# Performance work log

Hardware: AMD Instinct MI355X
Metric: run time of the kernel (lower is better)

## Reference

```python
import jax, jax.numpy as jnp
import numpy as np

H = 768          # MODEL_SIZE
N = 16           # SSM state modes (complex, conj-symmetric half)
NUM_LAYERS = 6
NUM_OUTS = 38


def setup_inputs() -> dict:
    key = jax.random.key(0)
    ks = jax.random.split(key, 24)
    B, L = 8, 2048
    scale = 0.02
    x_feat = jax.random.normal(ks[0], (B, L, 8), jnp.float32)
    x_raw = jax.random.normal(ks[1], (B, L, 8), jnp.float32)
    session_ids = jax.random.randint(ks[2], (B,), 0, 32)
    # encoder: Linear(8,H) -> Softsign -> Linear(H,H)
    enc_w1 = jax.random.normal(ks[3], (8, H), jnp.float32) * scale
    enc_b1 = jnp.zeros((H,), jnp.float32)
    enc_w2 = jax.random.normal(ks[4], (H, H), jnp.float32) * scale
    enc_b2 = jnp.zeros((H,), jnp.float32)
    # per-layer S4 params, stacked over NUM_LAYERS
    lo, hi = np.log(1e-3), np.log(1e-1)
    log_dt = lo + (hi - lo) * jax.random.uniform(ks[5], (NUM_LAYERS, H), jnp.float32)
    log_A_real = jnp.log(0.5 * jnp.ones((NUM_LAYERS, H, N), jnp.float32))
    A_imag = jnp.broadcast_to(np.pi * jnp.arange(N, dtype=jnp.float32), (NUM_LAYERS, H, N)) + 0.0
    C_ri = jax.random.normal(ks[6], (NUM_LAYERS, 2, H, N, 2), jnp.float32) * (0.5 ** 0.5)  # bidirectional C (re/im)
    D = jax.random.normal(ks[7], (NUM_LAYERS, H), jnp.float32)
    out_w = jax.random.normal(ks[8], (NUM_LAYERS, 2 * H, H), jnp.float32) * scale  # GLU output linear
    out_b = jnp.zeros((NUM_LAYERS, 2 * H), jnp.float32)
    norm_w = jnp.ones((NUM_LAYERS, H), jnp.float32)
    norm_b = jnp.zeros((NUM_LAYERS, H), jnp.float32)
    wout_w = jax.random.normal(ks[9], (H, NUM_OUTS), jnp.float32) * scale
    wout_b = jnp.zeros((NUM_OUTS,), jnp.float32)
    return dict(x_feat=x_feat, x_raw=x_raw, session_ids=session_ids,
                enc_w1=enc_w1, enc_b1=enc_b1, enc_w2=enc_w2, enc_b2=enc_b2,
                log_dt=log_dt, log_A_real=log_A_real, A_imag=A_imag, C_ri=C_ri,
                D=D, out_w=out_w, out_b=out_b, norm_w=norm_w, norm_b=norm_b,
                wout_w=wout_w, wout_b=wout_b)


def _s4_kernel(log_dt, log_A_real, A_imag, C_ri, L):
    """Bidirectional diagonal SSM conv kernel via ZOH discretization. Returns (2, H, L)."""
    dt = jnp.exp(log_dt)                              # (H,)
    A = (-jnp.exp(log_A_real) + 1j * A_imag).astype(jnp.complex64)   # (H, N)
    dtA = (dt[:, None] * A).astype(jnp.complex64)     # (H, N)
    dB = (jnp.exp(dtA) - 1.0) / A                     # ZOH input discretization (B=1)
    C = (C_ri[..., 0] + 1j * C_ri[..., 1]).astype(jnp.complex64)     # (2, H, N)
    vand = jnp.exp(dtA[:, :, None] * jnp.arange(L, dtype=jnp.float32))  # (H, N, L)
    K = 2.0 * jnp.einsum('chn,hnl->chl', C * dB, vand).real           # conj-symmetry factor
    return K.astype(jnp.float32)


def _s4_layer(x, log_dt, log_A_real, A_imag, C_ri, D, out_w, out_b, norm_w, norm_b):
    """x: (B, L, H) -> (B, L, H). Post-norm S4 block (eval mode, dropout=identity)."""
    B, L, _ = x.shape
    u = x.transpose(0, 2, 1)                          # (B, H, L)
    K = _s4_kernel(log_dt, log_A_real, A_imag, C_ri, L)  # (2, H, L)
    zpad = jnp.zeros((H, L), K.dtype)
    k = (jnp.concatenate([K[0], zpad], -1)
         + jnp.concatenate([zpad, jnp.flip(K[1], -1)], -1))            # (H, 2L) bidirectional kernel
    yf = jnp.fft.irfft(jnp.fft.rfft(u, n=2 * L) * jnp.fft.rfft(k, n=2 * L), n=2 * L)[..., :L]
    y = yf + D[:, None] * u                           # skip connection
    y = jax.nn.gelu(y, approximate=False)
    v = jnp.einsum('dh,bhl->bdl', out_w, y) + out_b[None, :, None]     # (B, 2H, L)
    a, g = jnp.split(v, 2, axis=1)
    z = a * jax.nn.sigmoid(g)                         # GLU
    xr = (z + u).transpose(0, 2, 1)                   # residual, back to (B, L, H)
    mu = xr.mean(-1, keepdims=True)
    var = ((xr - mu) ** 2).mean(-1, keepdims=True)
    return (xr - mu) / jnp.sqrt(var + 1e-5) * norm_w + norm_b          # post-LayerNorm


def reference(x_feat, x_raw, session_ids, enc_w1, enc_b1, enc_w2, enc_b2,
              log_dt, log_A_real, A_imag, C_ri, D, out_w, out_b,
              norm_w, norm_b, wout_w, wout_b):
    x = jax.nn.soft_sign(x_raw @ enc_w1 + enc_b1) @ enc_w2 + enc_b2    # encoder
    for i in range(NUM_LAYERS):
        x = _s4_layer(x, log_dt[i], log_A_real[i], A_imag[i], C_ri[i],
                      D[i], out_w[i], out_b[i], norm_w[i], norm_b[i])
        if i <= 2:
            x = x[:, ::2, :]                          # stride-2 downsample
    return x @ wout_w + wout_b                        # (B, L/8, num_outs)
```

## Files before the change

kernel.cpp:

```cpp
#include <hip/hip_runtime.h>
#include <hip/hip_bf16.h>
#include <math.h>

#define HDIM 768
#define NSTATE 16

typedef __attribute__((ext_vector_type(8))) short bf16x8;
typedef __attribute__((ext_vector_type(4))) float f32x4;
typedef __attribute__((ext_vector_type(4))) unsigned int u32x4;

__device__ __forceinline__ unsigned short f2bf(float f) {
    union { float f; unsigned int u; } v; v.f = f;
    unsigned int r = v.u + 0x7fff + ((v.u >> 16) & 1);
    return (unsigned short)(r >> 16);
}

__global__ void __launch_bounds__(256) wconv_kernel(
    const float* __restrict__ src, unsigned short* __restrict__ dst, int n8)
{
    int t = blockIdx.x * 256 + threadIdx.x;
    if (t >= n8) return;
    const float* s = src + (size_t)t * 8;
    float4 a = *(const float4*)s, b = *(const float4*)(s + 4);
    union { unsigned short us[8]; u32x4 v; } o;
    o.us[0] = f2bf(a.x); o.us[1] = f2bf(a.y); o.us[2] = f2bf(a.z); o.us[3] = f2bf(a.w);
    o.us[4] = f2bf(b.x); o.us[5] = f2bf(b.y); o.us[6] = f2bf(b.z); o.us[7] = f2bf(b.w);
    *(u32x4*)(dst + (size_t)t * 8) = o.v;
}

__global__ void __launch_bounds__(256) w2t_kernel(
    const float* __restrict__ w2, unsigned short* __restrict__ w2t)
{
    int T = blockIdx.x * 256 + threadIdx.x;
    int j = T / 96, kc = T - j * 96;
    union { unsigned short us[8]; u32x4 v; } o;
#pragma unroll
    for (int i = 0; i < 8; ++i)
        o.us[i] = f2bf(w2[(size_t)(kc * 8 + i) * HDIM + j]);
    *(u32x4*)(w2t + (size_t)j * HDIM + kc * 8) = o.v;
}

__global__ void __launch_bounds__(256) hprep_kernel(
    const float* __restrict__ xraw, const float* __restrict__ w1,
    const float* __restrict__ b1, unsigned short* __restrict__ hbf)
{
    __shared__ float w1s[8 * HDIM];
    __shared__ float b1s[HDIM];
    int tid = threadIdx.x;
    for (int p = tid; p < 8 * HDIM; p += 256) w1s[p] = w1[p];
    for (int p = tid; p < HDIM; p += 256) b1s[p] = b1[p];
    __syncthreads();
    int T = blockIdx.x * 256 + tid;
    int r = T / 96, kc = T - r * 96;
    float4 xa = *(const float4*)(xraw + (size_t)r * 8);
    float4 xb = *(const float4*)(xraw + (size_t)r * 8 + 4);
    float xq[8] = {xa.x, xa.y, xa.z, xa.w, xb.x, xb.y, xb.z, xb.w};
    float acc[8];
#pragma unroll
    for (int i = 0; i < 8; ++i) acc[i] = b1s[kc * 8 + i];
#pragma unroll
    for (int q = 0; q < 8; ++q)
#pragma unroll
        for (int i = 0; i < 8; ++i)
            acc[i] = fmaf(xq[q], w1s[q * HDIM + kc * 8 + i], acc[i]);
    union { unsigned short us[8]; u32x4 v; } o;
#pragma unroll
    for (int i = 0; i < 8; ++i) {
        float h = acc[i] / (1.0f + fabsf(acc[i]));
        o.us[i] = f2bf(h);
    }
    *(u32x4*)(hbf + (size_t)r * HDIM + kc * 8) = o.v;
}

__global__ void __launch_bounds__(256) enc_mfma_kernel(
    const unsigned short* __restrict__ w2t,
    const unsigned short* __restrict__ hbf,
    const float* __restrict__ b2,
    float* __restrict__ u0)
{
    __shared__ unsigned short lds[2][192 * 64];
    int tid = threadIdx.x;
    int j0 = blockIdx.x * 64;
    int r0 = blockIdx.y * 128;
    int w = tid >> 6, lane = tid & 63;
    int wj = w >> 1, wl = w & 1;
    f32x4 acc[2][4];
    f32x4 zf = {0.f, 0.f, 0.f, 0.f};
#pragma unroll
    for (int dg = 0; dg < 2; ++dg)
#pragma unroll
        for (int cg = 0; cg < 4; ++cg) acc[dg][cg] = zf;

    u32x4 stg[6];
#define ENC_LOAD(kt) do { int k0_ = (kt) * 64; \
    _Pragma("unroll") for (int s = 0; s < 6; ++s) { \
        int c = s * 256 + tid; int row = c >> 3, m = c & 7; \
        const unsigned short* g = (row < 64) \
            ? (w2t + (size_t)(j0 + row) * HDIM + k0_ + m * 8) \
            : (hbf + (size_t)(r0 + row - 64) * HDIM + k0_ + m * 8); \
        stg[s] = *(const u32x4*)g; } } while (0)
#define ENC_WRITE(bi) do { \
    _Pragma("unroll") for (int s = 0; s < 6; ++s) { \
        int c = s * 256 + tid; int row = c >> 3, m = c & 7; \
        *(u32x4*)&lds[bi][row * 64 + 8 * (m ^ (row & 7))] = stg[s]; } } while (0)

    ENC_LOAD(0); ENC_WRITE(0);
    int cur = 0;
    for (int t = 0; t < 12; ++t) {
        __syncthreads();
        if (t < 11) ENC_LOAD(t + 1);
#pragma unroll
        for (int kh = 0; kh < 2; ++kh) {
            int kg = kh * 4 + (lane >> 4);
            bf16x8 af[2], bfr[4];
#pragma unroll
            for (int dg = 0; dg < 2; ++dg) {
                int rA = wj * 32 + dg * 16 + (lane & 15);
                af[dg] = *(bf16x8*)&lds[cur][rA * 64 + 8 * (kg ^ (rA & 7))];
            }
#pragma unroll
            for (int cg = 0; cg < 4; ++cg) {
                int rB = 64 + wl * 64 + cg * 16 + (lane & 15);
                bfr[cg] = *(bf16x8*)&lds[cur][rB * 64 + 8 * (kg ^ (rB & 7))];
            }
#pragma unroll
            for (int dg = 0; dg < 2; ++dg)
#pragma unroll
                for (int cg = 0; cg < 4; ++cg)
                    acc[dg][cg] = __builtin_amdgcn_mfma_f32_16x16x32_bf16(
                        af[dg], bfr[cg], acc[dg][cg], 0, 0, 0);
        }
        if (t < 11) ENC_WRITE(cur ^ 1);
        cur ^= 1;
    }
    int b = r0 >> 11;
    int l0 = r0 & 2047;
#pragma unroll
    for (int dg = 0; dg < 2; ++dg) {
        int j = j0 + wj * 32 + dg * 16 + ((lane >> 4) << 2);
#pragma unroll
        for (int cg = 0; cg < 4; ++cg) {
            int l = l0 + wl * 64 + cg * 16 + (lane & 15);
#pragma unroll
            for (int i = 0; i < 4; ++i)
                u0[((size_t)(b * HDIM + j + i)) * 2048 + l] = acc[dg][cg][i] + b2[j + i];
        }
    }
#undef ENC_LOAD
#undef ENC_WRITE
}

__global__ void __launch_bounds__(256) glu_mfma_kernel(
    const unsigned short* __restrict__ wbf,
    const unsigned short* __restrict__ yt,
    const float* __restrict__ u,
    const float* __restrict__ ob,
    float* __restrict__ xr,
    int Lk, int ds)
{
    __shared__ unsigned short lds[2][256 * 64];
    int tid = threadIdx.x;
    int d0 = blockIdx.x * 64;
    int l0 = blockIdx.y * 128;
    int b  = blockIdx.z;
    int w = tid >> 6, lane = tid & 63;
    int wd = w >> 1, wl = w & 1;
    f32x4 accA[2][4], accG[2][4];
    f32x4 zf = {0.f, 0.f, 0.f, 0.f};
#pragma unroll
    for (int dg = 0; dg < 2; ++dg)
#pragma unroll
        for (int cg = 0; cg < 4; ++cg) { accA[dg][cg] = zf; accG[dg][cg] = zf; }

    u32x4 stg[8];
#define GLU_LOAD(kt) do { int k0_ = (kt) * 64; \
    _Pragma("unroll") for (int s = 0; s < 8; ++s) { \
        int c = s * 256 + tid; int row = c >> 3, m = c & 7; \
        const unsigned short* g; \
        if (row < 64)       g = wbf + (size_t)(d0 + row) * HDIM + k0_ + m * 8; \
        else if (row < 128) g = wbf + (size_t)(768 + d0 + row - 64) * HDIM + k0_ + m * 8; \
        else g = yt + ((size_t)b * Lk + l0 + row - 128) * HDIM + k0_ + m * 8; \
        stg[s] = *(const u32x4*)g; } } while (0)
#define GLU_WRITE(bi) do { \
    _Pragma("unroll") for (int s = 0; s < 8; ++s) { \
        int c = s * 256 + tid; int row = c >> 3, m = c & 7; \
        *(u32x4*)&lds[bi][row * 64 + 8 * (m ^ (row & 7))] = stg[s]; } } while (0)

    GLU_LOAD(0); GLU_WRITE(0);
    int cur = 0;
    for (int t = 0; t < 12; ++t) {
        __syncthreads();
        if (t < 11) GLU_LOAD(t + 1);
#pragma unroll
        for (int kh = 0; kh < 2; ++kh) {
            int kg = kh * 4 + (lane >> 4);
            bf16x8 aa[2], ag[2], bfr[4];
#pragma unroll
            for (int dg = 0; dg < 2; ++dg) {
                int rA = wd * 32 + dg * 16 + (lane & 15);
                aa[dg] = *(bf16x8*)&lds[cur][rA * 64 + 8 * (kg ^ (rA & 7))];
                int rG = 64 + rA;
                ag[dg] = *(bf16x8*)&lds[cur][rG * 64 + 8 * (kg ^ (rG & 7))];
            }
#pragma unroll
            for (int cg = 0; cg < 4; ++cg) {
                int rB = 128 + wl * 64 + cg * 16 + (lane & 15);
                bfr[cg] = *(bf16x8*)&lds[cur][rB * 64 + 8 * (kg ^ (rB & 7))];
            }
#pragma unroll
            for (int dg = 0; dg < 2; ++dg)
#pragma unroll
                for (int cg = 0; cg < 4; ++cg) {
                    accA[dg][cg] = __builtin_amdgcn_mfma_f32_16x16x32_bf16(
                        aa[dg], bfr[cg], accA[dg][cg], 0, 0, 0);
                    accG[dg][cg] = __builtin_amdgcn_mfma_f32_16x16x32_bf16(
                        ag[dg], bfr[cg], accG[dg][cg], 0, 0, 0);
                }
        }
        if (t < 11) GLU_WRITE(cur ^ 1);
        cur ^= 1;
    }
    size_t L = (size_t)Lk * ds;
#pragma unroll
    for (int dg = 0; dg < 2; ++dg) {
        int d = d0 + wd * 32 + dg * 16 + ((lane >> 4) << 2);
#pragma unroll
        for (int cg = 0; cg < 4; ++cg) {
            int l = l0 + wl * 64 + cg * 16 + (lane & 15);
#pragma unroll
            for (int i = 0; i < 4; ++i) {
                float a = accA[dg][cg][i] + ob[d + i];
                float g = accG[dg][cg][i] + ob[d + i + 768];
                float sg = 1.0f / (1.0f + expf(-g));
                float res = u[((size_t)b * HDIM + d + i) * L + (size_t)l * ds];
                xr[((size_t)b * HDIM + d + i) * Lk + l] = fmaf(a, sg, res);
            }
        }
    }
#undef GLU_LOAD
#undef GLU_WRITE
}

template<int DS>
__global__ void __launch_bounds__(256) ssm_split_kernel(
    const float* __restrict__ u,
    float* __restrict__ yout,
    const float* __restrict__ log_dt,
    const float* __restrict__ log_A_real,
    const float* __restrict__ A_imag,
    const float* __restrict__ C_ri,
    const float* __restrict__ Dp,
    int L, int lognch)
{
    __shared__ float4 tlsv[1024];
    const int KEPT = 32 / DS;
    int tid = threadIdx.x;
    int nch = 1 << lognch;
    int sh  = tid & 1;
    int j   = (tid >> 1) & (nch - 1);
    int rpb = 128 >> lognch;
    int lr  = tid >> (1 + lognch);
    int row = blockIdx.x * rpb + lr;
    int b   = row / HDIM;
    int h   = row - b * HDIM;
    int c0  = j * 32;
    const float* ur = u + (size_t)row * L;
    int Lk = L / DS;

    float zr[8], zi[8], zCr[8], zCi[8], w0r[8], w0i[8], w1r[8], w1i[8];
    float dt = expf(log_dt[h]);
#pragma unroll
    for (int k = 0; k < 8; ++k) {
        int n = sh * 8 + k;
        float Ar = -expf(log_A_real[h * NSTATE + n]);
        float Ai = A_imag[h * NSTATE + n];
        float er = expf(dt * Ar);
        float th = dt * Ai;
        zr[k] = er * cosf(th); zi[k] = er * sinf(th);
        float pr = zr[k], pi = zi[k];
#pragma unroll
        for (int s = 0; s < 5; ++s) {
            float t2 = pr * pr - pi * pi;
            pi = 2.f * pr * pi; pr = t2;
        }
        zCr[k] = pr; zCi[k] = pi;
        float den = Ar * Ar + Ai * Ai;
        float t0 = zr[k] - 1.0f;
        float dBr = (t0 * Ar + zi[k] * Ai) / den;
        float dBi = (zi[k] * Ar - t0 * Ai) / den;
        float C0r = C_ri[((0 * HDIM + h) * NSTATE + n) * 2 + 0];
        float C0i = C_ri[((0 * HDIM + h) * NSTATE + n) * 2 + 1];
        float C1r = C_ri[((1 * HDIM + h) * NSTATE + n) * 2 + 0];
        float C1i = C_ri[((1 * HDIM + h) * NSTATE + n) * 2 + 1];
        w0r[k] = 2.0f * (C0r * dBr - C0i * dBi);
        w0i[k] = 2.0f * (C0r * dBi + C0i * dBr);
        w1r[k] = 2.0f * (C1r * dBr - C1i * dBi);
        w1i[k] = 2.0f * (C1r * dBi + C1i * dBr);
    }
    int myslot = (j * rpb + lr) * 2 + sh;

    {
        float sr_[8] = {}, si_[8] = {};
#pragma unroll 8
        for (int i = 0; i < 32; ++i) {
            float uf = ur[c0 + i];
#pragma unroll
            for (int k = 0; k < 8; ++k) {
                float nr = fmaf(zr[k], sr_[k], fmaf(-zi[k], si_[k], uf));
                si_[k] = fmaf(zr[k], si_[k], zi[k] * sr_[k]);
                sr_[k] = nr;
            }
        }
#pragma unroll
        for (int q = 0; q < 4; ++q)
            tlsv[myslot * 4 + (q ^ (myslot & 3))] =
                make_float4(sr_[2 * q], si_[2 * q], sr_[2 * q + 1], si_[2 * q + 1]);
    }
    __syncthreads();

    float Sr[8] = {}, Si[8] = {};
    for (int i = 0; i < j; ++i) {
        int sl = (i * rpb + lr) * 2 + sh;
        float4 t0v = tlsv[sl * 4 + (0 ^ (sl & 3))];
        float4 t1v = tlsv[sl * 4 + (1 ^ (sl & 3))];
        float4 t2v = tlsv[sl * 4 + (2 ^ (sl & 3))];
        float4 t3v = tlsv[sl * 4 + (3 ^ (sl & 3))];
        float tr[8] = {t0v.x, t0v.z, t1v.x, t1v.z, t2v.x, t2v.z, t3v.x, t3v.z};
        float ti[8] = {t0v.y, t0v.w, t1v.y, t1v.w, t2v.y, t2v.w, t3v.y, t3v.w};
#pragma unroll
        for (int k = 0; k < 8; ++k) {
            float nr = fmaf(zCr[k], Sr[k], fmaf(-zCi[k], Si[k], tr[k]));
            Si[k] = fmaf(zCr[k], Si[k], fmaf(zCi[k], Sr[k], ti[k]));
            Sr[k] = nr;
        }
    }

    float Dh_eff = (sh == 0) ? Dp[h] : 0.0f;
    float cf[KEPT];
#pragma unroll
    for (int i = 0; i < 32; ++i) {
        float uf = ur[c0 + i];
        float ca = 0.f, cb = 0.f;
#pragma unroll
        for (int k = 0; k < 8; ++k) {
            float nr = fmaf(zr[k], Sr[k], fmaf(-zi[k], Si[k], uf));
            Si[k] = fmaf(zr[k], Si[k], zi[k] * Sr[k]);
            Sr[k] = nr;
            float c = fmaf(w0r[k], Sr[k], -w0i[k] * Si[k]);
            if (k & 1) cb += c; else ca += c;
        }
        if ((i & (DS - 1)) == 0)
            cf[i / DS] = fmaf(Dh_eff, uf, ca + cb);
    }
    __syncthreads();

    {
        float sr_[8] = {}, si_[8] = {};
#pragma unroll 8
        for (int m = 0; m < 32; ++m) {
            int idx = c0 + 32 - m;
            float ub = (idx < L) ? ur[idx] : 0.f;
#pragma unroll
            for (int k = 0; k < 8; ++k) {
                float nr = fmaf(zr[k], sr_[k], fmaf(-zi[k], si_[k], ub));
                si_[k] = fmaf(zr[k], si_[k], zi[k] * sr_[k]);
                sr_[k] = nr;
            }
        }
#pragma unroll
        for (int q = 0; q < 4; ++q)
            tlsv[myslot * 4 + (q ^ (myslot & 3))] =
                make_float4(sr_[2 * q], si_[2 * q], sr_[2 * q + 1], si_[2 * q + 1]);
    }
    __syncthreads();

    float Er[8] = {}, Ei[8] = {};
    for (int i = nch - 1; i > j; --i) {
        int sl = (i * rpb + lr) * 2 + sh;
        float4 t0v = tlsv[sl * 4 + (0 ^ (sl & 3))];
        float4 t1v = tlsv[sl * 4 + (1 ^ (sl & 3))];
        float4 t2v = tlsv[sl * 4 + (2 ^ (sl & 3))];
        float4 t3v = tlsv[sl * 4 + (3 ^ (sl & 3))];
        float tr[8] = {t0v.x, t0v.z, t1v.x, t1v.z, t2v.x, t2v.z, t3v.x, t3v.z};
        float ti[8] = {t0v.y, t0v.w, t1v.y, t1v.w, t2v.y, t2v.w, t3v.y, t3v.w};
#pragma unroll
        for (int k = 0; k < 8; ++k) {
            float nr = fmaf(zCr[k], Er[k], fmaf(-zCi[k], Ei[k], tr[k]));
            Ei[k] = fmaf(zCr[k], Ei[k], fmaf(zCi[k], Er[k], ti[k]));
            Er[k] = nr;
        }
    }

    float* yr = yout + (size_t)row * Lk + (c0 / DS);
#pragma unroll
    for (int m = 0; m < 32; ++m) {
        int idx = c0 + 32 - m;
        float ub = (idx < L) ? ur[idx] : 0.f;
#pragma unroll
        for (int k = 0; k < 8; ++k) {
            float nr = fmaf(zr[k], Er[k], fmaf(-zi[k], Ei[k], ub));
            Ei[k] = fmaf(zr[k], Ei[k], zi[k] * Er[k]);
            Er[k] = nr;
        }
        if (((31 - m) & (DS - 1)) == 0) {
            float ca = 0.f, cb = 0.f;
#pragma unroll
            for (int k = 0; k < 8; ++k) {
                float c = fmaf(w1r[k], Er[k], -w1i[k] * Ei[k]);
                if (k & 1) cb += c; else ca += c;
            }
            int k2 = (31 - m) / DS;
            float v = cf[k2] + ca + cb;
            v += __shfl_xor(v, 1, 64);
            if (sh == 0) {
                float g = 0.5f * v * (1.0f + erff(v * 0.70710678118f));
                yr[k2] = g;
            }
        }
    }
}

__global__ void __launch_bounds__(256) ytr_kernel(
    const float* __restrict__ yf, unsigned short* __restrict__ yt, int Lk)
{
    __shared__ float tile[64][65];
    int tid = threadIdx.x;
    int p0 = blockIdx.x * 64;
    int r0 = blockIdx.y * 64;
    int tp = tid & 63, th = tid >> 6;
#pragma unroll
    for (int s = 0; s < 16; ++s) {
        int hh = th * 16 + s;
        tile[hh][tp] = yf[(size_t)(r0 + hh) * Lk + p0 + tp];
    }
    __syncthreads();
    int b = r0 / HDIM, h0 = r0 - b * HDIM;
#pragma unroll
    for (int s = 0; s < 16; ++s) {
        int pp = th * 16 + s;
        yt[((size_t)b * Lk + p0 + pp) * HDIM + h0 + tp] = f2bf(tile[tp][pp]);
    }
}

__global__ void __launch_bounds__(256) ln_kernel(
    const float* __restrict__ x, float* __restrict__ dst,
    const float* __restrict__ nw, const float* __restrict__ nb, int Lk)
{
    __shared__ float ss[16][17], qq[16][17], mus[16], rss[16];
    int tid = threadIdx.x;
    int lo = tid & 15, hg = tid >> 4;
    int b = blockIdx.y;
    int l = blockIdx.x * 16 + lo;
    const float* base = x + (size_t)b * HDIM * Lk + l;
    float s = 0.f, q = 0.f;
    for (int hh = hg; hh < HDIM; hh += 16) {
        float v = base[(size_t)hh * Lk];
        s += v; q = fmaf(v, v, q);
    }
    ss[hg][lo] = s; qq[hg][lo] = q;
    __syncthreads();
    if (hg == 0) {
        float S = 0.f, Q = 0.f;
#pragma unroll
        for (int t2 = 0; t2 < 16; ++t2) { S += ss[t2][lo]; Q += qq[t2][lo]; }
        float mu = S * (1.0f / HDIM);
        float var = Q * (1.0f / HDIM) - mu * mu;
        mus[lo] = mu; rss[lo] = rsqrtf(var + 1e-5f);
    }
    __syncthreads();
    float mu = mus[lo], rs = rss[lo];
    float* dbase = dst + (size_t)b * HDIM * Lk + l;
    for (int hh = hg; hh < HDIM; hh += 16) {
        float v = base[(size_t)hh * Lk];
        dbase[(size_t)hh * Lk] = (v - mu) * rs * nw[hh] + nb[hh];
    }
}

__global__ void __launch_bounds__(256) head_kernel(
    const float* __restrict__ u, const float* __restrict__ wout,
    const float* __restrict__ wb, float* __restrict__ out, int Lk)
{
    __shared__ float us[64][68];
    __shared__ float wsh[64][40];
    int tid = threadIdx.x;
    int lt = tid & 63, og = tid >> 6;
    int b = blockIdx.y;
    int l0 = blockIdx.x * 64;
    int ur_ = tid >> 2, uq = tid & 3;
    float acc[10];
#pragma unroll
    for (int k = 0; k < 10; ++k) acc[k] = 0.f;

    for (int c0 = 0; c0 < HDIM; c0 += 64) {
        for (int p = tid; p < 64 * 38; p += 256) {
            int hh = p / 38, o = p - hh * 38;
            wsh[hh][o] = wout[(size_t)(c0 + hh) * 38 + o];
        }
        {
            const float* gr = u + ((size_t)b * HDIM + c0 + ur_) * Lk + l0;
            float4 v0 = *(const float4*)(gr + (uq + 0) * 4);
            float4 v1 = *(const float4*)(gr + (uq + 4) * 4);
            float4 v2 = *(const float4*)(gr + (uq + 8) * 4);
            float4 v3 = *(const float4*)(gr + (uq + 12) * 4);
            *(float4*)&us[ur_][(uq + 0) * 4] = v0;
            *(float4*)&us[ur_][(uq + 4) * 4] = v1;
            *(float4*)&us[ur_][(uq + 8) * 4] = v2;
            *(float4*)&us[ur_][(uq + 12) * 4] = v3;
        }
        __syncthreads();
#pragma unroll 8
        for (int hh = 0; hh < 64; ++hh) {
            float uv = us[hh][lt];
#pragma unroll
            for (int k = 0; k < 10; ++k) {
                int o = og + 4 * k;
                if (o < 38) acc[k] = fmaf(uv, wsh[hh][o], acc[k]);
            }
        }
        __syncthreads();
    }
#pragma unroll
    for (int k = 0; k < 10; ++k) {
        int o = og + 4 * k;
        if (o < 38)
            out[((size_t)b * Lk + l0 + lt) * 38 + o] = acc[k] + wb[o];
    }
}

extern "C" void kernel_launch(void* const* d_in, const int* in_sizes, int n_in,
                              void* d_out, int out_size, void* d_ws, size_t ws_size,
                              hipStream_t stream)
{
    (void)in_sizes; (void)n_in; (void)out_size; (void)ws_size;
    const float* x_raw      = (const float*)d_in[1];
    const float* enc_w1     = (const float*)d_in[3];
    const float* enc_b1     = (const float*)d_in[4];
    const float* enc_w2     = (const float*)d_in[5];
    const float* enc_b2     = (const float*)d_in[6];
    const float* log_dt     = (const float*)d_in[7];
    const float* log_A_real = (const float*)d_in[8];
    const float* A_imag     = (const float*)d_in[9];
    const float* C_ri       = (const float*)d_in[10];
    const float* Dp         = (const float*)d_in[11];
    const float* out_w      = (const float*)d_in[12];
    const float* out_b      = (const float*)d_in[13];
    const float* norm_w     = (const float*)d_in[14];
    const float* norm_b     = (const float*)d_in[15];
    const float* wout_w     = (const float*)d_in[16];
    const float* wout_b     = (const float*)d_in[17];

    char* ws = (char*)d_ws;
    float* Abuf = (float*)ws;
    char*  Bb   = ws + 50331648;
    unsigned short* hbf   = (unsigned short*)Bb;
    unsigned short* ytb   = (unsigned short*)Bb;
    unsigned short* wslot = (unsigned short*)(Bb + 12582912);
    char*  Cb   = ws + 75497472;
    unsigned short* w2t = (unsigned short*)Cb;
    float* yf = (float*)Cb;
    float* xr = (float*)Cb;

    const int B = 8;

    w2t_kernel<<<288, 256, 0, stream>>>(enc_w2, w2t);
    hprep_kernel<<<6144, 256, 0, stream>>>(x_raw, enc_w1, enc_b1, hbf);
    enc_mfma_kernel<<<dim3(12, 128), 256, 0, stream>>>(w2t, hbf, enc_b2, Abuf);

    int L = 2048;
    for (int i = 0; i < 6; ++i) {
        int ds = (i <= 2) ? 2 : 1;
        int Lk = L / ds;
        int lognch = 31 - __builtin_clz(L / 32);
        int rpb = 128 >> lognch;
        int nblk = 6144 / rpb;
        if (ds == 2)
            ssm_split_kernel<2><<<nblk, 256, 0, stream>>>(
                Abuf, yf,
                log_dt + (size_t)i * HDIM,
                log_A_real + (size_t)i * HDIM * NSTATE,
                A_imag + (size_t)i * HDIM * NSTATE,
                C_ri + (size_t)i * 2 * HDIM * NSTATE * 2,
                Dp + (size_t)i * HDIM, L, lognch);
        else
            ssm_split_kernel<1><<<nblk, 256, 0, stream>>>(
                Abuf, yf,
                log_dt + (size_t)i * HDIM,
                log_A_real + (size_t)i * HDIM * NSTATE,
                A_imag + (size_t)i * HDIM * NSTATE,
                C_ri + (size_t)i * 2 * HDIM * NSTATE * 2,
                Dp + (size_t)i * HDIM, L, lognch);
        ytr_kernel<<<dim3(Lk / 64, 96), 256, 0, stream>>>(yf, ytb, Lk);
        wconv_kernel<<<576, 256, 0, stream>>>(
            out_w + (size_t)i * 1536 * HDIM, wslot, 1536 * 96);
        glu_mfma_kernel<<<dim3(12, Lk / 128, B), 256, 0, stream>>>(
            wslot, ytb, Abuf, out_b + (size_t)i * 1536, xr, Lk, ds);
        ln_kernel<<<dim3(Lk / 16, B), 256, 0, stream>>>(
            xr, Abuf, norm_w + (size_t)i * HDIM, norm_b + (size_t)i * HDIM, Lk);
        L = Lk;
    }

    head_kernel<<<dim3(L / 64, B), 256, 0, stream>>>(
        Abuf, wout_w, wout_b, (float*)d_out, L);
}
```

Measured before the change: 1.243 ms.

## Replace serial chunk-carry loop with log-step parallel scan in SSM kernel

The sequential O(nch) loop over preceding and following chunk states, used to build the carry-in for each chunk, is replaced by a Hillis-Steele style prefix scan in shared memory that takes lognch steps with squared decay powers. Each step adds a pair of block barriers. Separately, the C-projection in the forward pass is now computed only at kept (downsampled) positions instead of at every step. The scan adds synchronisation overhead and changes floating-point summation order in exchange for fewer serial chunk steps.

```diff
diff --git a/kernel.cpp b/kernel.cpp
--- a/kernel.cpp
+++ b/kernel.cpp
@@ -242,7 +242,7 @@
 }
 
 template<int DS>
-__global__ void __launch_bounds__(256) ssm_split_kernel(
+__global__ void __launch_bounds__(256) ssm_scan_kernel(
     const float* __restrict__ u,
     float* __restrict__ yout,
     const float* __restrict__ log_dt,
@@ -299,6 +299,21 @@
     }
     int myslot = (j * rpb + lr) * 2 + sh;
 
+#define SLOT_WRITE(RR, II) do { \
+    _Pragma("unroll") for (int q = 0; q < 4; ++q) \
+        tlsv[myslot * 4 + (q ^ (myslot & 3))] = \
+            make_float4(RR[2 * q], II[2 * q], RR[2 * q + 1], II[2 * q + 1]); } while (0)
+#define SLOT_READ(SL, RR, II) do { int sl_ = (SL); \
+    float4 a0 = tlsv[sl_ * 4 + (0 ^ (sl_ & 3))]; \
+    float4 a1 = tlsv[sl_ * 4 + (1 ^ (sl_ & 3))]; \
+    float4 a2 = tlsv[sl_ * 4 + (2 ^ (sl_ & 3))]; \
+    float4 a3 = tlsv[sl_ * 4 + (3 ^ (sl_ & 3))]; \
+    RR[0] = a0.x; II[0] = a0.y; RR[1] = a0.z; II[1] = a0.w; \
+    RR[2] = a1.x; II[2] = a1.y; RR[3] = a1.z; II[3] = a1.w; \
+    RR[4] = a2.x; II[4] = a2.y; RR[5] = a2.z; II[5] = a2.w; \
+    RR[6] = a3.x; II[6] = a3.y; RR[7] = a3.z; II[7] = a3.w; } while (0)
+
+    float Pr[8], Pi[8];
     {
         float sr_[8] = {}, si_[8] = {};
 #pragma unroll 8
@@ -312,45 +327,60 @@
             }
         }
 #pragma unroll
-        for (int q = 0; q < 4; ++q)
-            tlsv[myslot * 4 + (q ^ (myslot & 3))] =
-                make_float4(sr_[2 * q], si_[2 * q], sr_[2 * q + 1], si_[2 * q + 1]);
-    }
+        for (int k = 0; k < 8; ++k) { Pr[k] = sr_[k]; Pi[k] = si_[k]; }
+    }
+    SLOT_WRITE(Pr, Pi);
     __syncthreads();
 
+    {
+        float wkr[8], wki[8];
+#pragma unroll
+        for (int k = 0; k < 8; ++k) { wkr[k] = zCr[k]; wki[k] = zCi[k]; }
+        for (int st = 0; st < lognch; ++st) {
+            int pj = j - (1 << st);
+            float tr[8], ti[8];
+            bool act = (pj >= 0);
+            if (act) SLOT_READ((pj * rpb + lr) * 2 + sh, tr, ti);
+            __syncthreads();
+            if (act) {
+#pragma unroll
+                for (int k = 0; k < 8; ++k) {
+                    Pr[k] = fmaf(wkr[k], tr[k], fmaf(-wki[k], ti[k], Pr[k]));
+                    Pi[k] = fmaf(wkr[k], ti[k], fmaf(wki[k], tr[k], Pi[k]));
+                }
+            }
+            SLOT_WRITE(Pr, Pi);
+            __syncthreads();
+#pragma unroll
+            for (int k = 0; k < 8; ++k) {
+                float t2 = wkr[k] * wkr[k] - wki[k] * wki[k];
+                wki[k] = 2.f * wkr[k] * wki[k]; wkr[k] = t2;
+            }
+        }
+    }
     float Sr[8] = {}, Si[8] = {};
-    for (int i = 0; i < j; ++i) {
-        int sl = (i * rpb + lr) * 2 + sh;
-        float4 t0v = tlsv[sl * 4 + (0 ^ (sl & 3))];
-        float4 t1v = tlsv[sl * 4 + (1 ^ (sl & 3))];
-        float4 t2v = tlsv[sl * 4 + (2 ^ (sl & 3))];
-        float4 t3v = tlsv[sl * 4 + (3 ^ (sl & 3))];
-        float tr[8] = {t0v.x, t0v.z, t1v.x, t1v.z, t2v.x, t2v.z, t3v.x, t3v.z};
-        float ti[8] = {t0v.y, t0v.w, t1v.y, t1v.w, t2v.y, t2v.w, t3v.y, t3v.w};
-#pragma unroll
-        for (int k = 0; k < 8; ++k) {
-            float nr = fmaf(zCr[k], Sr[k], fmaf(-zCi[k], Si[k], tr[k]));
-            Si[k] = fmaf(zCr[k], Si[k], fmaf(zCi[k], Sr[k], ti[k]));
-            Sr[k] = nr;
-        }
-    }
+    if (j > 0) SLOT_READ(((j - 1) * rpb + lr) * 2 + sh, Sr, Si);
 
     float Dh_eff = (sh == 0) ? Dp[h] : 0.0f;
     float cf[KEPT];
 #pragma unroll
     for (int i = 0; i < 32; ++i) {
         float uf = ur[c0 + i];
-        float ca = 0.f, cb = 0.f;
 #pragma unroll
         for (int k = 0; k < 8; ++k) {
             float nr = fmaf(zr[k], Sr[k], fmaf(-zi[k], Si[k], uf));
             Si[k] = fmaf(zr[k], Si[k], zi[k] * Sr[k]);
             Sr[k] = nr;
-            float c = fmaf(w0r[k], Sr[k], -w0i[k] * Si[k]);
-            if (k & 1) cb += c; else ca += c;
-        }
-        if ((i & (DS - 1)) == 0)
+        }
+        if ((i & (DS - 1)) == 0) {
+            float ca = 0.f, cb = 0.f;
+#pragma unroll
+            for (int k = 0; k < 8; ++k) {
+                float c = fmaf(w0r[k], Sr[k], -w0i[k] * Si[k]);
+                if (k & 1) cb += c; else ca += c;
+            }
             cf[i / DS] = fmaf(Dh_eff, uf, ca + cb);
+        }
     }
     __syncthreads();
 
@@ -368,28 +398,39 @@
             }
         }
 #pragma unroll
-        for (int q = 0; q < 4; ++q)
-            tlsv[myslot * 4 + (q ^ (myslot & 3))] =
-                make_float4(sr_[2 * q], si_[2 * q], sr_[2 * q + 1], si_[2 * q + 1]);
-    }
+        for (int k = 0; k < 8; ++k) { Pr[k] = sr_[k]; Pi[k] = si_[k]; }
+    }
+    SLOT_WRITE(Pr, Pi);
     __syncthreads();
 
+    {
+        float wkr[8], wki[8];
+#pragma unroll
+        for (int k = 0; k < 8; ++k) { wkr[k] = zCr[k]; wki[k] = zCi[k]; }
+        for (int st = 0; st < lognch; ++st) {
+            int pj = j + (1 << st);
+            float tr[8], ti[8];
+            bool act = (pj < nch);
+            if (act) SLOT_READ((pj * rpb + lr) * 2 + sh, tr, ti);
+            __syncthreads();
+            if (act) {
+#pragma unroll
+                for (int k = 0; k < 8; ++k) {
+                    Pr[k] = fmaf(wkr[k], tr[k], fmaf(-wki[k], ti[k], Pr[k]));
+                    Pi[k] = fmaf(wkr[k], ti[k], fmaf(wki[k], tr[k], Pi[k]));
+                }
+            }
+            SLOT_WRITE(Pr, Pi);
+            __syncthreads();
+#pragma unroll
+            for (int k = 0; k < 8; ++k) {
+                float t2 = wkr[k] * wkr[k] - wki[k] * wki[k];
+                wki[k] = 2.f * wkr[k] * wki[k]; wkr[k] = t2;
+            }
+        }
+    }
     float Er[8] = {}, Ei[8] = {};
-    for (int i = nch - 1; i > j; --i) {
-        int sl = (i * rpb + lr) * 2 + sh;
-        float4 t0v = tlsv[sl * 4 + (0 ^ (sl & 3))];
-        float4 t1v = tlsv[sl * 4 + (1 ^ (sl & 3))];
-        float4 t2v = tlsv[sl * 4 + (2 ^ (sl & 3))];
-        float4 t3v = tlsv[sl * 4 + (3 ^ (sl & 3))];
-        float tr[8] = {t0v.x, t0v.z, t1v.x, t1v.z, t2v.x, t2v.z, t3v.x, t3v.z};
-        float ti[8] = {t0v.y, t0v.w, t1v.y, t1v.w, t2v.y, t2v.w, t3v.y, t3v.w};
-#pragma unroll
-        for (int k = 0; k < 8; ++k) {
-            float nr = fmaf(zCr[k], Er[k], fmaf(-zCi[k], Ei[k], tr[k]));
-            Ei[k] = fmaf(zCr[k], Ei[k], fmaf(zCi[k], Er[k], ti[k]));
-            Er[k] = nr;
-        }
-    }
+    if (j < nch - 1) SLOT_READ(((j + 1) * rpb + lr) * 2 + sh, Er, Ei);
 
     float* yr = yout + (size_t)row * Lk + (c0 / DS);
 #pragma unroll
@@ -418,6 +459,8 @@
             }
         }
     }
+#undef SLOT_WRITE
+#undef SLOT_READ
 }
 
 __global__ void __launch_bounds__(256) ytr_kernel(
@@ -574,7 +617,7 @@
         int rpb = 128 >> lognch;
         int nblk = 6144 / rpb;
         if (ds == 2)
-            ssm_split_kernel<2><<<nblk, 256, 0, stream>>>(
+            ssm_scan_kernel<2><<<nblk, 256, 0, stream>>>(
                 Abuf, yf,
                 log_dt + (size_t)i * HDIM,
                 log_A_real + (size_t)i * HDIM * NSTATE,
@@ -582,7 +625,7 @@
                 C_ri + (size_t)i * 2 * HDIM * NSTATE * 2,
                 Dp + (size_t)i * HDIM, L, lognch);
         else
-            ssm_split_kernel<1><<<nblk, 256, 0, stream>>>(
+            ssm_scan_kernel<1><<<nblk, 256, 0, stream>>>(
                 Abuf, yf,
                 log_dt + (size_t)i * HDIM,
                 log_A_real + (size_t)i * HDIM * NSTATE,
```

Result: faster. 1.196 ms (-3.8%).
